# Kernel optimization log

Measured on AMD Instinct MI355X. Metric: run time of the kernel, lower is better.

The kernel has to match this reference:

```python
import jax, jax.numpy as jnp
import numpy as np

N_NODES = 50000
N_EDGES = 800000
D_IN = 96
D_OUT = 96
N_GRAPHS = 50


def setup_inputs() -> dict:
    key = jax.random.key(0)
    ks = jax.random.split(key, 16)
    s = 1.0 / np.sqrt(D_IN)
    inp = {
        "x": jax.random.normal(ks[0], (N_NODES, D_IN), jnp.float32),
        "edge_index": jax.random.randint(ks[1], (2, N_EDGES), 0, N_NODES, jnp.int32),
        "edge_attr": jax.random.uniform(ks[2], (N_EDGES, 1), jnp.float32),
        "batch": jnp.sort(jax.random.randint(ks[3], (N_NODES,), 0, N_GRAPHS, jnp.int32)),
        "w1_w": jax.random.normal(ks[4], (D_IN, D_OUT), jnp.float32) * s,
        "w1_b": jax.random.normal(ks[5], (D_OUT,), jnp.float32) * 0.01,
        "w2_w": jax.random.normal(ks[6], (D_IN, D_OUT), jnp.float32) * s,
        "w2_b": jax.random.normal(ks[7], (D_OUT,), jnp.float32) * 0.01,
        "w3_w": jax.random.normal(ks[8], (D_IN, D_OUT), jnp.float32) * s,
        "w3_b": jax.random.normal(ks[9], (D_OUT,), jnp.float32) * 0.01,
        "w4_w": jax.random.normal(ks[10], (D_IN, D_OUT), jnp.float32) * s,
        "w4_b": jax.random.normal(ks[11], (D_OUT,), jnp.float32) * 0.01,
        "w5_w": jax.random.normal(ks[12], (1, D_OUT), jnp.float32),
        "w5_b": jax.random.normal(ks[13], (D_OUT,), jnp.float32) * 0.01,
    }
    return inp


def reference(x, edge_index, edge_attr, batch,
              w1_w, w1_b, w2_w, w2_b, w3_w, w3_b, w4_w, w4_b, w5_w, w5_b):
    n = x.shape[0]
    src, dst = edge_index[0], edge_index[1]  # x_j = x[src], x_i = x[dst]
    sqrt_d = jnp.sqrt(jnp.asarray(D_OUT, x.dtype))

    x_i = x[dst]                                  # [E, D]
    x_j = x[src]                                  # [E, D]
    xi_t = x_i @ w3_w + w3_b                      # w3(x_i)
    xj_t = x_j @ w4_w + w4_b                      # w4(x_j)
    ea_t = edge_attr @ w5_w + w5_b                # w5(edge_attr), [E, D]

    scores = jnp.sum(xi_t * (xj_t + ea_t), axis=-1) / sqrt_d  # [E]

    # segment softmax over destination-node neighborhoods (PyG softmax)
    seg_max = jax.ops.segment_max(scores, dst, num_segments=n)
    ex = jnp.exp(scores - seg_max[dst])
    denom = jax.ops.segment_sum(ex, dst, num_segments=n)
    alpha = ex / (denom[dst] + jnp.asarray(1e-16, x.dtype))

    msg = alpha[:, None] * (x_j @ w2_w + w2_b)    # [E, D]
    aggr = jax.ops.segment_sum(msg, dst, num_segments=n)

    node_out = x @ w1_w + w1_b + aggr             # update: w1(x) + aggr

    # global mean pool per graph
    sums = jax.ops.segment_sum(node_out, batch, num_segments=N_GRAPHS)
    counts = jax.ops.segment_sum(jnp.ones((n,), x.dtype), batch, num_segments=N_GRAPHS)
    return sums / jnp.maximum(counts, 1.0)[:, None]
```

## Files before the change

### kernel.cpp

```cpp
#include <hip/hip_runtime.h>
#include <math.h>

#define D 96
#define RSQ 0.10206207261596577f
#define TSTRIDE 104

typedef __attribute__((ext_vector_type(8))) short short8;
typedef __attribute__((ext_vector_type(4))) float f32x4;

__device__ __forceinline__ unsigned short f2bf(float f){
  unsigned u = __float_as_uint(f);
  unsigned r = (u + 0x7fff + ((u >> 16) & 1)) >> 16;
  return (unsigned short)r;
}
__device__ __forceinline__ float bf2f(unsigned short h){
  return __uint_as_float(((unsigned)h) << 16);
}
__device__ __forceinline__ float bflo(unsigned u){ return __uint_as_float(u << 16); }
__device__ __forceinline__ float bfhi(unsigned u){ return __uint_as_float(u & 0xffff0000u); }
__device__ __forceinline__ int lbound(const int* __restrict__ a, int n, int v){
  int lo = 0, hi = n;
  while (lo < hi){ int mid = (lo + hi) >> 1; if (a[mid] < v) lo = mid + 1; else hi = mid; }
  return lo;
}

__global__ __launch_bounds__(256) void k_wprep_deg(
    const float* __restrict__ w1, const float* __restrict__ w2,
    const float* __restrict__ w3, const float* __restrict__ w4,
    unsigned short* __restrict__ wt_h, unsigned short* __restrict__ wt_l,
    const int* __restrict__ dstI, int* __restrict__ deg, int E){
  int gtid = blockIdx.x * 256 + threadIdx.x;
  if (gtid < 4 * D * D){
    int m = gtid / (D * D);
    int r = gtid % (D * D);
    int nn = r / D, k = r % D;
    const float* w = (m == 0) ? w1 : (m == 1) ? w2 : (m == 2) ? w3 : w4;
    float v = w[k * D + nn];
    unsigned short h = f2bf(v);
    wt_h[gtid] = h;
    wt_l[gtid] = f2bf(v - bf2f(h));
  }
  if (gtid < E) atomicAdd(&deg[dstI[gtid]], 1);
}

__global__ __launch_bounds__(256) void k_transform_mfma(
    const float* __restrict__ x,
    const unsigned short* __restrict__ wt_h, const unsigned short* __restrict__ wt_l,
    const float* __restrict__ b1, const float* __restrict__ b2,
    const float* __restrict__ b3, const float* __restrict__ b4,
    const float* __restrict__ w5, const float* __restrict__ b5,
    float* __restrict__ acc_o, unsigned short* __restrict__ x2o,
    float* __restrict__ x3o, unsigned short* __restrict__ x4o,
    float* __restrict__ p5, float* __restrict__ pb, int n){
  __shared__ __align__(16) unsigned short xs_h[16][TSTRIDE];
  __shared__ __align__(16) unsigned short xs_l[16][TSTRIDE];
  int tid = threadIdx.x;
  int n0 = blockIdx.x * 16;
  for (int e = tid; e < 16 * D; e += 256){
    int r = e / D, c = e % D;
    int node = n0 + r;
    float v = (node < n) ? x[(size_t)node * D + c] : 0.0f;
    unsigned short h = f2bf(v);
    xs_h[r][c] = h;
    xs_l[r][c] = f2bf(v - bf2f(h));
  }
  __syncthreads();

  int wv = tid >> 6;
  int lane = tid & 63;
  int lr = lane & 15;
  int kg = lane >> 4;

  f32x4 acc0 = {0,0,0,0}, acc1 = {0,0,0,0}, acc2 = {0,0,0,0};
  f32x4 acc3 = {0,0,0,0}, acc4 = {0,0,0,0}, acc5 = {0,0,0,0};
  const unsigned short* wtm_h = wt_h + (size_t)wv * D * D;
  const unsigned short* wtm_l = wt_l + (size_t)wv * D * D;

  #pragma unroll
  for (int k0 = 0; k0 < D; k0 += 32){
    int kb = k0 + kg * 8;
    short8 ah = *(const short8*)&xs_h[lr][kb];
    short8 al = *(const short8*)&xs_l[lr][kb];
    #pragma unroll
    for (int nc = 0; nc < 6; ++nc){
      int col = nc * 16 + lr;
      short8 bh = *(const short8*)(wtm_h + col * D + kb);
      short8 bl = *(const short8*)(wtm_l + col * D + kb);
      f32x4 a = (nc == 0) ? acc0 : (nc == 1) ? acc1 : (nc == 2) ? acc2
              : (nc == 3) ? acc3 : (nc == 4) ? acc4 : acc5;
      a = __builtin_amdgcn_mfma_f32_16x16x32_bf16(ah, bh, a, 0, 0, 0);
      a = __builtin_amdgcn_mfma_f32_16x16x32_bf16(ah, bl, a, 0, 0, 0);
      a = __builtin_amdgcn_mfma_f32_16x16x32_bf16(al, bh, a, 0, 0, 0);
      if (nc == 0) acc0 = a; else if (nc == 1) acc1 = a; else if (nc == 2) acc2 = a;
      else if (nc == 3) acc3 = a; else if (nc == 4) acc4 = a; else acc5 = a;
    }
  }

  const float* bias = (wv == 0) ? b1 : (wv == 1) ? b2 : (wv == 2) ? b3 : b4;
  float p5p0 = 0, p5p1 = 0, p5p2 = 0, p5p3 = 0;
  float pbp0 = 0, pbp1 = 0, pbp2 = 0, pbp3 = 0;
  #pragma unroll
  for (int nc = 0; nc < 6; ++nc){
    int col = nc * 16 + lr;
    float bb = bias[col];
    float w5v = w5[col], b5v = b5[col];
    f32x4 a = (nc == 0) ? acc0 : (nc == 1) ? acc1 : (nc == 2) ? acc2
            : (nc == 3) ? acc3 : (nc == 4) ? acc4 : acc5;
    #pragma unroll
    for (int q = 0; q < 4; ++q){
      float v = a[q] + bb;
      int row = kg * 4 + q;
      if (n0 + row < n){
        size_t o = (size_t)(n0 + row) * D + col;
        if (wv == 0) acc_o[o] = v;
        else if (wv == 1) x2o[o] = f2bf(v);
        else if (wv == 2) x3o[o] = v;
        else x4o[o] = f2bf(v);
      }
      float t5 = v * w5v, tb = v * b5v;
      if (q == 0){ p5p0 += t5; pbp0 += tb; }
      else if (q == 1){ p5p1 += t5; pbp1 += tb; }
      else if (q == 2){ p5p2 += t5; pbp2 += tb; }
      else { p5p3 += t5; pbp3 += tb; }
    }
  }
  if (wv == 2){
    #pragma unroll
    for (int off = 1; off < 16; off <<= 1){
      p5p0 += __shfl_xor(p5p0, off); pbp0 += __shfl_xor(pbp0, off);
      p5p1 += __shfl_xor(p5p1, off); pbp1 += __shfl_xor(pbp1, off);
      p5p2 += __shfl_xor(p5p2, off); pbp2 += __shfl_xor(pbp2, off);
      p5p3 += __shfl_xor(p5p3, off); pbp3 += __shfl_xor(pbp3, off);
    }
    if (lr == 0){
      int row = kg * 4;
      if (n0 + row < n)     { p5[n0 + row]     = p5p0; pb[n0 + row]     = pbp0; }
      if (n0 + row + 1 < n) { p5[n0 + row + 1] = p5p1; pb[n0 + row + 1] = pbp1; }
      if (n0 + row + 2 < n) { p5[n0 + row + 2] = p5p2; pb[n0 + row + 2] = pbp2; }
      if (n0 + row + 3 < n) { p5[n0 + row + 3] = p5p3; pb[n0 + row + 3] = pbp3; }
    }
  }
}

__global__ __launch_bounds__(256) void k_scanA(
    const int* __restrict__ deg, int* __restrict__ rowp,
    int* __restrict__ partials, int n){
  __shared__ int ws[4];
  int tid = threadIdx.x, lane = tid & 63, wid = tid >> 6;
  int i = blockIdx.x * 256 + tid;
  int v = (i < n) ? deg[i] : 0;
  int s = v;
  #pragma unroll
  for (int off = 1; off < 64; off <<= 1){ int u = __shfl_up(s, off); if (lane >= off) s += u; }
  if (lane == 63) ws[wid] = s;
  __syncthreads();
  if (tid < 4){
    int u = ws[tid];
    #pragma unroll
    for (int off = 1; off < 4; off <<= 1){ int q = __shfl_up(u, off); if (tid >= off) u += q; }
    ws[tid] = u;
  }
  __syncthreads();
  int woff = wid ? ws[wid - 1] : 0;
  if (i < n) rowp[i] = woff + s - v;
  if (tid == 255) partials[blockIdx.x] = ws[3];
}

__global__ __launch_bounds__(256) void k_scanB(
    int* __restrict__ partials, int* __restrict__ rowp, int nb, int n){
  __shared__ int ws[4];
  int tid = threadIdx.x, lane = tid & 63, wid = tid >> 6;
  int running = 0;
  for (int base = 0; base < nb; base += 256){
    int i = base + tid;
    int v = (i < nb) ? partials[i] : 0;
    int s = v;
    #pragma unroll
    for (int off = 1; off < 64; off <<= 1){ int u = __shfl_up(s, off); if (lane >= off) s += u; }
    if (lane == 63) ws[wid] = s;
    __syncthreads();
    if (tid < 4){
      int u = ws[tid];
      #pragma unroll
      for (int off = 1; off < 4; off <<= 1){ int q = __shfl_up(u, off); if (tid >= off) u += q; }
      ws[tid] = u;
    }
    __syncthreads();
    int woff = wid ? ws[wid - 1] : 0;
    if (i < nb) partials[i] = running + woff + s - v;
    running += ws[3];
    __syncthreads();
  }
  if (tid == 0) rowp[n] = running;
}

__global__ __launch_bounds__(256) void k_scatter(
    const int* __restrict__ srcI, const int* __restrict__ dstI,
    const float* __restrict__ eattr, const int* __restrict__ rowp,
    const int* __restrict__ partials, int* __restrict__ fill,
    int2* __restrict__ sortedSE, int E){
  int e = blockIdx.x * blockDim.x + threadIdx.x;
  if (e >= E) return;
  int t = dstI[e];
  int pos = rowp[t] + partials[t >> 8] + atomicAdd(&fill[t], 1);
  sortedSE[pos] = make_int2(srcI[e], __float_as_int(eattr[e]));
}

__global__ __launch_bounds__(256) void k_attn(
    const unsigned short* __restrict__ x2b, const float* __restrict__ x3,
    const unsigned short* __restrict__ x4b, const float* __restrict__ p5,
    const float* __restrict__ pb, const int2* __restrict__ sortedSE,
    const int* __restrict__ rowp, const int* __restrict__ partials,
    float* __restrict__ node_acc, int n){
  int t = blockIdx.x * 4 + (threadIdx.x >> 6);
  int lane = threadIdx.x & 63;
  if (t >= n) return;
  int beg = rowp[t] + partials[t >> 8];
  int end = (t + 1 < n) ? (rowp[t + 1] + partials[(t + 1) >> 8]) : rowp[n];
  if (beg == end) return;
  int j = lane & 15;
  int g = lane >> 4;

  const float2* r3 = (const float2*)(x3 + (size_t)t * D);
  float2 v0 = r3[j], v1 = r3[j + 16], v2 = r3[j + 32];
  float p5t = p5[t], pbt = pb[t];

  float m = -INFINITY, dsum = 0.0f;
  float a0 = 0, a1 = 0, a2 = 0, a3 = 0, a4 = 0, a5 = 0;

  for (int c = beg; c < end; c += 8){
    int eA = c + g, eB = c + 4 + g;
    bool actA = eA < end, actB = eB < end;
    int2 seA = sortedSE[actA ? eA : end - 1];
    int2 seB = sortedSE[actB ? eB : end - 1];
    const unsigned* r4A = (const unsigned*)(x4b + (size_t)seA.x * D);
    const unsigned* r4B = (const unsigned*)(x4b + (size_t)seB.x * D);
    unsigned uA0 = r4A[j], uA1 = r4A[j + 16], uA2 = r4A[j + 32];
    unsigned uB0 = r4B[j], uB1 = r4B[j + 16], uB2 = r4B[j + 32];
    float sA = v0.x * bflo(uA0) + v0.y * bfhi(uA0)
             + v1.x * bflo(uA1) + v1.y * bfhi(uA1)
             + v2.x * bflo(uA2) + v2.y * bfhi(uA2);
    float sB = v0.x * bflo(uB0) + v0.y * bfhi(uB0)
             + v1.x * bflo(uB1) + v1.y * bfhi(uB1)
             + v2.x * bflo(uB2) + v2.y * bfhi(uB2);
    sA += __shfl_xor(sA, 1); sA += __shfl_xor(sA, 2);
    sA += __shfl_xor(sA, 4); sA += __shfl_xor(sA, 8);
    sB += __shfl_xor(sB, 1); sB += __shfl_xor(sB, 2);
    sB += __shfl_xor(sB, 4); sB += __shfl_xor(sB, 8);
    float scA = actA ? (sA + __int_as_float(seA.y) * p5t + pbt) * RSQ : -INFINITY;
    float scB = actB ? (sB + __int_as_float(seB.y) * p5t + pbt) * RSQ : -INFINITY;
    float mc = fmaxf(scA, scB);
    mc = fmaxf(mc, __shfl_xor(mc, 16));
    mc = fmaxf(mc, __shfl_xor(mc, 32));
    if (mc > m){
      float r = __expf(m - mc);
      dsum *= r; a0 *= r; a1 *= r; a2 *= r; a3 *= r; a4 *= r; a5 *= r;
      m = mc;
    }
    float wA = __expf(scA - m);
    float wB = __expf(scB - m);
    dsum += wA + wB;
    const unsigned* r2A = (const unsigned*)(x2b + (size_t)seA.x * D);
    const unsigned* r2B = (const unsigned*)(x2b + (size_t)seB.x * D);
    unsigned qA0 = r2A[j], qA1 = r2A[j + 16], qA2 = r2A[j + 32];
    unsigned qB0 = r2B[j], qB1 = r2B[j + 16], qB2 = r2B[j + 32];
    a0 += wA * bflo(qA0) + wB * bflo(qB0);
    a1 += wA * bfhi(qA0) + wB * bfhi(qB0);
    a2 += wA * bflo(qA1) + wB * bflo(qB1);
    a3 += wA * bfhi(qA1) + wB * bfhi(qB1);
    a4 += wA * bflo(qA2) + wB * bflo(qB2);
    a5 += wA * bfhi(qA2) + wB * bfhi(qB2);
  }
  a0 += __shfl_xor(a0, 16); a0 += __shfl_xor(a0, 32);
  a1 += __shfl_xor(a1, 16); a1 += __shfl_xor(a1, 32);
  a2 += __shfl_xor(a2, 16); a2 += __shfl_xor(a2, 32);
  a3 += __shfl_xor(a3, 16); a3 += __shfl_xor(a3, 32);
  a4 += __shfl_xor(a4, 16); a4 += __shfl_xor(a4, 32);
  a5 += __shfl_xor(a5, 16); a5 += __shfl_xor(a5, 32);
  dsum += __shfl_xor(dsum, 16); dsum += __shfl_xor(dsum, 32);
  float inv = 1.0f / (dsum + 1e-16f);
  if (lane < 16){
    size_t o = (size_t)t * D + 2 * j;
    node_acc[o]      += a0 * inv;
    node_acc[o + 1]  += a1 * inv;
    node_acc[o + 32] += a2 * inv;
    node_acc[o + 33] += a3 * inv;
    node_acc[o + 64] += a4 * inv;
    node_acc[o + 65] += a5 * inv;
  }
}

__global__ __launch_bounds__(96) void k_pool(
    const float* __restrict__ node_out, const int* __restrict__ batch,
    float* __restrict__ sums, int n){
  int g = blockIdx.x;
  int chunk = blockIdx.y, nch = gridDim.y;
  int lo = lbound(batch, n, g);
  int hi = lbound(batch, n, g + 1);
  int cnt = hi - lo;
  if (cnt <= 0) return;
  int per = (cnt + nch - 1) / nch;
  int b = lo + chunk * per;
  int e = min(b + per, hi);
  if (b >= e) return;
  int d = threadIdx.x;
  float s = 0.0f;
  for (int r = b; r < e; ++r) s += node_out[(size_t)r * D + d];
  atomicAdd(&sums[g * D + d], s);
}

__global__ __launch_bounds__(256) void k_final(
    const float* __restrict__ sums, const int* __restrict__ batch,
    float* __restrict__ out, int n, int total){
  int i = blockIdx.x * blockDim.x + threadIdx.x;
  if (i >= total) return;
  int g = i / D;
  int lo = lbound(batch, n, g);
  int hi = lbound(batch, n, g + 1);
  float c = (float)((hi - lo) > 1 ? (hi - lo) : 1);
  out[i] = sums[i] / c;
}

extern "C" void kernel_launch(void* const* d_in, const int* in_sizes, int n_in,
                              void* d_out, int out_size, void* d_ws, size_t ws_size,
                              hipStream_t stream){
  const float* x     = (const float*)d_in[0];
  const int*   eidx  = (const int*)d_in[1];
  const float* eattr = (const float*)d_in[2];
  const int*   batch = (const int*)d_in[3];
  const float* w1 = (const float*)d_in[4];
  const float* b1 = (const float*)d_in[5];
  const float* w2 = (const float*)d_in[6];
  const float* b2 = (const float*)d_in[7];
  const float* w3 = (const float*)d_in[8];
  const float* b3 = (const float*)d_in[9];
  const float* w4 = (const float*)d_in[10];
  const float* b4 = (const float*)d_in[11];
  const float* w5 = (const float*)d_in[12];
  const float* b5 = (const float*)d_in[13];
  float* out = (float*)d_out;

  const int N = in_sizes[0] / D;
  const int E = in_sizes[2];
  const int* srcI = eidx;
  const int* dstI = eidx + E;
  const int NB = (N + 255) / 256;

  char* base = (char*)d_ws;
  size_t off = 0;
  auto alloc = [&](size_t bytes) -> char* {
    char* p = base + off;
    off = (off + bytes + 255) & ~(size_t)255;
    return p;
  };
  char* zbase = base;
  int*   deg   = (int*)alloc((size_t)N * 4);
  int*   fill  = (int*)alloc((size_t)N * 4);
  float* sums  = (float*)alloc((size_t)out_size * 4);
  size_t zbytes = off;
  float* node_acc = (float*)alloc((size_t)N * D * 4);
  unsigned short* x2v = (unsigned short*)alloc((size_t)N * D * 2);
  float* x3v      = (float*)alloc((size_t)N * D * 4);
  unsigned short* x4v = (unsigned short*)alloc((size_t)N * D * 2);
  float* p5       = (float*)alloc((size_t)N * 4);
  float* pb       = (float*)alloc((size_t)N * 4);
  int*   rowp     = (int*)alloc((size_t)(N + 1) * 4);
  int*   partials = (int*)alloc((size_t)(NB + 1) * 4);
  int2*  sortedSE = (int2*)alloc((size_t)E * 8);
  unsigned short* wt_h = (unsigned short*)alloc((size_t)4 * D * D * 2);
  unsigned short* wt_l = (unsigned short*)alloc((size_t)4 * D * D * 2);
  (void)ws_size; (void)n_in;

  hipMemsetAsync(zbase, 0, zbytes, stream);

  k_wprep_deg<<<dim3((E + 255) / 256), dim3(256), 0, stream>>>(
      w1, w2, w3, w4, wt_h, wt_l, dstI, deg, E);
  k_transform_mfma<<<dim3((N + 15) / 16), dim3(256), 0, stream>>>(
      x, wt_h, wt_l, b1, b2, b3, b4, w5, b5,
      node_acc, x2v, x3v, x4v, p5, pb, N);
  k_scanA<<<dim3(NB), dim3(256), 0, stream>>>(deg, rowp, partials, N);
  k_scanB<<<dim3(1), dim3(256), 0, stream>>>(partials, rowp, NB, N);
  k_scatter<<<dim3((E + 255) / 256), dim3(256), 0, stream>>>(
      srcI, dstI, eattr, rowp, partials, fill, sortedSE, E);
  k_attn<<<dim3((N + 3) / 4), dim3(256), 0, stream>>>(
      x2v, x3v, x4v, p5, pb, sortedSE, rowp, partials, node_acc, N);
  k_pool<<<dim3(out_size / D, 32), dim3(D), 0, stream>>>(node_acc, batch, sums, N);
  k_final<<<dim3((out_size + 255) / 256), dim3(256), 0, stream>>>(
      sums, batch, out, N, out_size);
}
```

Before: 302.3 us.

## Interleave x4/x2 rows, reuse degree-count rank in scatter, 32-row transform tiles

Stores the bf16 w4 and w2 projections side by side in one 192-wide row, so the attention kernel's gathers of x4 and x2 for each source node hit adjacent memory. The rank returned by the degree-counting atomicAdd is saved and reused in the scatter, which removes the second atomic pass and the fill buffer. The transform kernel now processes 32 nodes per block, so each weight fragment load feeds two row tiles. In exchange it adds an E-sized rank buffer and more accumulator registers in the transform kernel.

```diff
diff --git a/kernel.cpp b/kernel.cpp
--- a/kernel.cpp
+++ b/kernel.cpp
@@ -28,7 +28,8 @@
     const float* __restrict__ w1, const float* __restrict__ w2,
     const float* __restrict__ w3, const float* __restrict__ w4,
     unsigned short* __restrict__ wt_h, unsigned short* __restrict__ wt_l,
-    const int* __restrict__ dstI, int* __restrict__ deg, int E){
+    const int* __restrict__ dstI, int* __restrict__ deg,
+    int* __restrict__ rank, int E){
   int gtid = blockIdx.x * 256 + threadIdx.x;
   if (gtid < 4 * D * D){
     int m = gtid / (D * D);
@@ -40,7 +41,7 @@
     wt_h[gtid] = h;
     wt_l[gtid] = f2bf(v - bf2f(h));
   }
-  if (gtid < E) atomicAdd(&deg[dstI[gtid]], 1);
+  if (gtid < E) rank[gtid] = atomicAdd(&deg[dstI[gtid]], 1);
 }
 
 __global__ __launch_bounds__(256) void k_transform_mfma(
@@ -49,14 +50,14 @@
     const float* __restrict__ b1, const float* __restrict__ b2,
     const float* __restrict__ b3, const float* __restrict__ b4,
     const float* __restrict__ w5, const float* __restrict__ b5,
-    float* __restrict__ acc_o, unsigned short* __restrict__ x2o,
-    float* __restrict__ x3o, unsigned short* __restrict__ x4o,
+    float* __restrict__ acc_o, unsigned short* __restrict__ x24,
+    float* __restrict__ x3o,
     float* __restrict__ p5, float* __restrict__ pb, int n){
-  __shared__ __align__(16) unsigned short xs_h[16][TSTRIDE];
-  __shared__ __align__(16) unsigned short xs_l[16][TSTRIDE];
+  __shared__ __align__(16) unsigned short xs_h[32][TSTRIDE];
+  __shared__ __align__(16) unsigned short xs_l[32][TSTRIDE];
   int tid = threadIdx.x;
-  int n0 = blockIdx.x * 16;
-  for (int e = tid; e < 16 * D; e += 256){
+  int n0 = blockIdx.x * 32;
+  for (int e = tid; e < 32 * D; e += 256){
     int r = e / D, c = e % D;
     int node = n0 + r;
     float v = (node < n) ? x[(size_t)node * D + c] : 0.0f;
@@ -71,73 +72,83 @@
   int lr = lane & 15;
   int kg = lane >> 4;
 
-  f32x4 acc0 = {0,0,0,0}, acc1 = {0,0,0,0}, acc2 = {0,0,0,0};
-  f32x4 acc3 = {0,0,0,0}, acc4 = {0,0,0,0}, acc5 = {0,0,0,0};
+  f32x4 c00 = {0,0,0,0}, c01 = {0,0,0,0}, c02 = {0,0,0,0};
+  f32x4 c03 = {0,0,0,0}, c04 = {0,0,0,0}, c05 = {0,0,0,0};
+  f32x4 c10 = {0,0,0,0}, c11 = {0,0,0,0}, c12 = {0,0,0,0};
+  f32x4 c13 = {0,0,0,0}, c14 = {0,0,0,0}, c15 = {0,0,0,0};
   const unsigned short* wtm_h = wt_h + (size_t)wv * D * D;
   const unsigned short* wtm_l = wt_l + (size_t)wv * D * D;
 
   #pragma unroll
   for (int k0 = 0; k0 < D; k0 += 32){
     int kb = k0 + kg * 8;
-    short8 ah = *(const short8*)&xs_h[lr][kb];
-    short8 al = *(const short8*)&xs_l[lr][kb];
-    #pragma unroll
-    for (int nc = 0; nc < 6; ++nc){
-      int col = nc * 16 + lr;
-      short8 bh = *(const short8*)(wtm_h + col * D + kb);
-      short8 bl = *(const short8*)(wtm_l + col * D + kb);
-      f32x4 a = (nc == 0) ? acc0 : (nc == 1) ? acc1 : (nc == 2) ? acc2
-              : (nc == 3) ? acc3 : (nc == 4) ? acc4 : acc5;
-      a = __builtin_amdgcn_mfma_f32_16x16x32_bf16(ah, bh, a, 0, 0, 0);
-      a = __builtin_amdgcn_mfma_f32_16x16x32_bf16(ah, bl, a, 0, 0, 0);
-      a = __builtin_amdgcn_mfma_f32_16x16x32_bf16(al, bh, a, 0, 0, 0);
-      if (nc == 0) acc0 = a; else if (nc == 1) acc1 = a; else if (nc == 2) acc2 = a;
-      else if (nc == 3) acc3 = a; else if (nc == 4) acc4 = a; else acc5 = a;
-    }
+    short8 ah0 = *(const short8*)&xs_h[lr][kb];
+    short8 al0 = *(const short8*)&xs_l[lr][kb];
+    short8 ah1 = *(const short8*)&xs_h[lr + 16][kb];
+    short8 al1 = *(const short8*)&xs_l[lr + 16][kb];
+    #define NC_BODY(nc, C0, C1) { \
+      int col = (nc) * 16 + lr; \
+      short8 bh = *(const short8*)(wtm_h + col * D + kb); \
+      short8 bl = *(const short8*)(wtm_l + col * D + kb); \
+      C0 = __builtin_amdgcn_mfma_f32_16x16x32_bf16(ah0, bh, C0, 0, 0, 0); \
+      C0 = __builtin_amdgcn_mfma_f32_16x16x32_bf16(ah0, bl, C0, 0, 0, 0); \
+      C0 = __builtin_amdgcn_mfma_f32_16x16x32_bf16(al0, bh, C0, 0, 0, 0); \
+      C1 = __builtin_amdgcn_mfma_f32_16x16x32_bf16(ah1, bh, C1, 0, 0, 0); \
+      C1 = __builtin_amdgcn_mfma_f32_16x16x32_bf16(ah1, bl, C1, 0, 0, 0); \
+      C1 = __builtin_amdgcn_mfma_f32_16x16x32_bf16(al1, bh, C1, 0, 0, 0); }
+    NC_BODY(0, c00, c10) NC_BODY(1, c01, c11) NC_BODY(2, c02, c12)
+    NC_BODY(3, c03, c13) NC_BODY(4, c04, c14) NC_BODY(5, c05, c15)
+    #undef NC_BODY
   }
 
   const float* bias = (wv == 0) ? b1 : (wv == 1) ? b2 : (wv == 2) ? b3 : b4;
-  float p5p0 = 0, p5p1 = 0, p5p2 = 0, p5p3 = 0;
-  float pbp0 = 0, pbp1 = 0, pbp2 = 0, pbp3 = 0;
-  #pragma unroll
-  for (int nc = 0; nc < 6; ++nc){
-    int col = nc * 16 + lr;
-    float bb = bias[col];
-    float w5v = w5[col], b5v = b5[col];
-    f32x4 a = (nc == 0) ? acc0 : (nc == 1) ? acc1 : (nc == 2) ? acc2
-            : (nc == 3) ? acc3 : (nc == 4) ? acc4 : acc5;
-    #pragma unroll
-    for (int q = 0; q < 4; ++q){
-      float v = a[q] + bb;
-      int row = kg * 4 + q;
-      if (n0 + row < n){
-        size_t o = (size_t)(n0 + row) * D + col;
-        if (wv == 0) acc_o[o] = v;
-        else if (wv == 1) x2o[o] = f2bf(v);
-        else if (wv == 2) x3o[o] = v;
-        else x4o[o] = f2bf(v);
-      }
-      float t5 = v * w5v, tb = v * b5v;
-      if (q == 0){ p5p0 += t5; pbp0 += tb; }
-      else if (q == 1){ p5p1 += t5; pbp1 += tb; }
-      else if (q == 2){ p5p2 += t5; pbp2 += tb; }
-      else { p5p3 += t5; pbp3 += tb; }
-    }
-  }
+  f32x4 p5a0 = {0,0,0,0}, p5a1 = {0,0,0,0};
+  f32x4 pba0 = {0,0,0,0}, pba1 = {0,0,0,0};
+
+  #define EPI_BODY(nc, C0, C1) { \
+    int col = (nc) * 16 + lr; \
+    float bb = bias[col]; \
+    float w5v = w5[col], b5v = b5[col]; \
+    _Pragma("unroll") \
+    for (int q = 0; q < 4; ++q){ \
+      float v0e = C0[q] + bb; \
+      float v1e = C1[q] + bb; \
+      int row0 = kg * 4 + q, row1 = 16 + kg * 4 + q; \
+      if (n0 + row0 < n){ \
+        if (wv == 0) acc_o[(size_t)(n0 + row0) * D + col] = v0e; \
+        else if (wv == 1) x24[(size_t)(n0 + row0) * 192 + 96 + col] = f2bf(v0e); \
+        else if (wv == 2) x3o[(size_t)(n0 + row0) * D + col] = v0e; \
+        else x24[(size_t)(n0 + row0) * 192 + col] = f2bf(v0e); \
+      } \
+      if (n0 + row1 < n){ \
+        if (wv == 0) acc_o[(size_t)(n0 + row1) * D + col] = v1e; \
+        else if (wv == 1) x24[(size_t)(n0 + row1) * 192 + 96 + col] = f2bf(v1e); \
+        else if (wv == 2) x3o[(size_t)(n0 + row1) * D + col] = v1e; \
+        else x24[(size_t)(n0 + row1) * 192 + col] = f2bf(v1e); \
+      } \
+      p5a0[q] += v0e * w5v; pba0[q] += v0e * b5v; \
+      p5a1[q] += v1e * w5v; pba1[q] += v1e * b5v; \
+    } }
+  EPI_BODY(0, c00, c10) EPI_BODY(1, c01, c11) EPI_BODY(2, c02, c12)
+  EPI_BODY(3, c03, c13) EPI_BODY(4, c04, c14) EPI_BODY(5, c05, c15)
+  #undef EPI_BODY
+
   if (wv == 2){
     #pragma unroll
     for (int off = 1; off < 16; off <<= 1){
-      p5p0 += __shfl_xor(p5p0, off); pbp0 += __shfl_xor(pbp0, off);
-      p5p1 += __shfl_xor(p5p1, off); pbp1 += __shfl_xor(pbp1, off);
-      p5p2 += __shfl_xor(p5p2, off); pbp2 += __shfl_xor(pbp2, off);
-      p5p3 += __shfl_xor(p5p3, off); pbp3 += __shfl_xor(pbp3, off);
+      #pragma unroll
+      for (int q = 0; q < 4; ++q){
+        p5a0[q] += __shfl_xor(p5a0[q], off); pba0[q] += __shfl_xor(pba0[q], off);
+        p5a1[q] += __shfl_xor(p5a1[q], off); pba1[q] += __shfl_xor(pba1[q], off);
+      }
     }
     if (lr == 0){
-      int row = kg * 4;
-      if (n0 + row < n)     { p5[n0 + row]     = p5p0; pb[n0 + row]     = pbp0; }
-      if (n0 + row + 1 < n) { p5[n0 + row + 1] = p5p1; pb[n0 + row + 1] = pbp1; }
-      if (n0 + row + 2 < n) { p5[n0 + row + 2] = p5p2; pb[n0 + row + 2] = pbp2; }
-      if (n0 + row + 3 < n) { p5[n0 + row + 3] = p5p3; pb[n0 + row + 3] = pbp3; }
+      #pragma unroll
+      for (int q = 0; q < 4; ++q){
+        int row0 = kg * 4 + q, row1 = 16 + kg * 4 + q;
+        if (n0 + row0 < n){ p5[n0 + row0] = p5a0[q]; pb[n0 + row0] = pba0[q]; }
+        if (n0 + row1 < n){ p5[n0 + row1] = p5a1[q]; pb[n0 + row1] = pba1[q]; }
+      }
     }
   }
 }
@@ -197,18 +208,18 @@
 __global__ __launch_bounds__(256) void k_scatter(
     const int* __restrict__ srcI, const int* __restrict__ dstI,
     const float* __restrict__ eattr, const int* __restrict__ rowp,
-    const int* __restrict__ partials, int* __restrict__ fill,
+    const int* __restrict__ partials, const int* __restrict__ rank,
     int2* __restrict__ sortedSE, int E){
   int e = blockIdx.x * blockDim.x + threadIdx.x;
   if (e >= E) return;
   int t = dstI[e];
-  int pos = rowp[t] + partials[t >> 8] + atomicAdd(&fill[t], 1);
+  int pos = rowp[t] + partials[t >> 8] + rank[e];
   sortedSE[pos] = make_int2(srcI[e], __float_as_int(eattr[e]));
 }
 
 __global__ __launch_bounds__(256) void k_attn(
-    const unsigned short* __restrict__ x2b, const float* __restrict__ x3,
-    const unsigned short* __restrict__ x4b, const float* __restrict__ p5,
+    const unsigned short* __restrict__ x24, const float* __restrict__ x3,
+    const float* __restrict__ p5,
     const float* __restrict__ pb, const int2* __restrict__ sortedSE,
     const int* __restrict__ rowp, const int* __restrict__ partials,
     float* __restrict__ node_acc, int n){
@@ -233,10 +244,10 @@
     bool actA = eA < end, actB = eB < end;
     int2 seA = sortedSE[actA ? eA : end - 1];
     int2 seB = sortedSE[actB ? eB : end - 1];
-    const unsigned* r4A = (const unsigned*)(x4b + (size_t)seA.x * D);
-    const unsigned* r4B = (const unsigned*)(x4b + (size_t)seB.x * D);
-    unsigned uA0 = r4A[j], uA1 = r4A[j + 16], uA2 = r4A[j + 32];
-    unsigned uB0 = r4B[j], uB1 = r4B[j + 16], uB2 = r4B[j + 32];
+    const unsigned* rA = (const unsigned*)(x24 + (size_t)seA.x * 192);
+    const unsigned* rB = (const unsigned*)(x24 + (size_t)seB.x * 192);
+    unsigned uA0 = rA[j], uA1 = rA[j + 16], uA2 = rA[j + 32];
+    unsigned uB0 = rB[j], uB1 = rB[j + 16], uB2 = rB[j + 32];
     float sA = v0.x * bflo(uA0) + v0.y * bfhi(uA0)
              + v1.x * bflo(uA1) + v1.y * bfhi(uA1)
              + v2.x * bflo(uA2) + v2.y * bfhi(uA2);
@@ -260,10 +271,8 @@
     float wA = __expf(scA - m);
     float wB = __expf(scB - m);
     dsum += wA + wB;
-    const unsigned* r2A = (const unsigned*)(x2b + (size_t)seA.x * D);
-    const unsigned* r2B = (const unsigned*)(x2b + (size_t)seB.x * D);
-    unsigned qA0 = r2A[j], qA1 = r2A[j + 16], qA2 = r2A[j + 32];
-    unsigned qB0 = r2B[j], qB1 = r2B[j + 16], qB2 = r2B[j + 32];
+    unsigned qA0 = rA[48 + j], qA1 = rA[48 + j + 16], qA2 = rA[48 + j + 32];
+    unsigned qB0 = rB[48 + j], qB1 = rB[48 + j + 16], qB2 = rB[48 + j + 32];
     a0 += wA * bflo(qA0) + wB * bflo(qB0);
     a1 += wA * bfhi(qA0) + wB * bfhi(qB0);
     a2 += wA * bflo(qA1) + wB * bflo(qB1);
@@ -345,6 +354,7 @@
   const int* srcI = eidx;
   const int* dstI = eidx + E;
   const int NB = (N + 255) / 256;
+  const int NT = (N + 31) / 32;
 
   char* base = (char*)d_ws;
   size_t off = 0;
@@ -355,17 +365,16 @@
   };
   char* zbase = base;
   int*   deg   = (int*)alloc((size_t)N * 4);
-  int*   fill  = (int*)alloc((size_t)N * 4);
   float* sums  = (float*)alloc((size_t)out_size * 4);
   size_t zbytes = off;
   float* node_acc = (float*)alloc((size_t)N * D * 4);
-  unsigned short* x2v = (unsigned short*)alloc((size_t)N * D * 2);
+  unsigned short* x24 = (unsigned short*)alloc((size_t)N * 192 * 2);
   float* x3v      = (float*)alloc((size_t)N * D * 4);
-  unsigned short* x4v = (unsigned short*)alloc((size_t)N * D * 2);
   float* p5       = (float*)alloc((size_t)N * 4);
   float* pb       = (float*)alloc((size_t)N * 4);
   int*   rowp     = (int*)alloc((size_t)(N + 1) * 4);
   int*   partials = (int*)alloc((size_t)(NB + 1) * 4);
+  int*   rank     = (int*)alloc((size_t)E * 4);
   int2*  sortedSE = (int2*)alloc((size_t)E * 8);
   unsigned short* wt_h = (unsigned short*)alloc((size_t)4 * D * D * 2);
   unsigned short* wt_l = (unsigned short*)alloc((size_t)4 * D * D * 2);
@@ -374,16 +383,16 @@
   hipMemsetAsync(zbase, 0, zbytes, stream);
 
   k_wprep_deg<<<dim3((E + 255) / 256), dim3(256), 0, stream>>>(
-      w1, w2, w3, w4, wt_h, wt_l, dstI, deg, E);
-  k_transform_mfma<<<dim3((N + 15) / 16), dim3(256), 0, stream>>>(
+      w1, w2, w3, w4, wt_h, wt_l, dstI, deg, rank, E);
+  k_transform_mfma<<<dim3(NT), dim3(256), 0, stream>>>(
       x, wt_h, wt_l, b1, b2, b3, b4, w5, b5,
-      node_acc, x2v, x3v, x4v, p5, pb, N);
+      node_acc, x24, x3v, p5, pb, N);
   k_scanA<<<dim3(NB), dim3(256), 0, stream>>>(deg, rowp, partials, N);
   k_scanB<<<dim3(1), dim3(256), 0, stream>>>(partials, rowp, NB, N);
   k_scatter<<<dim3((E + 255) / 256), dim3(256), 0, stream>>>(
-      srcI, dstI, eattr, rowp, partials, fill, sortedSE, E);
+      srcI, dstI, eattr, rowp, partials, rank, sortedSE, E);
   k_attn<<<dim3((N + 3) / 4), dim3(256), 0, stream>>>(
-      x2v, x3v, x4v, p5, pb, sortedSE, rowp, partials, node_acc, N);
+      x24, x3v, p5, pb, sortedSE, rowp, partials, node_acc, N);
   k_pool<<<dim3(out_size / D, 32), dim3(D), 0, stream>>>(node_acc, batch, sums, N);
   k_final<<<dim3((out_size + 255) / 256), dim3(256), 0, stream>>>(
       sums, batch, out, N, out_size);
```

Measured after the change: 273.2 us. 9.6% less time.
